# Kernel optimization log

Hardware: AMD Instinct MI355X
Metric: run time of the kernel (lower is better)

The kernel has to match this reference:

```python
import jax, jax.numpy as jnp
import numpy as np

D = 32          # latent_dimension
N = 100000      # num nodes
E = 3200000     # num edges (avg degree 32)
K = 4           # message-passing steps
GAMMA = 0.9
ALPHA = 0.5


def _lin(key, out_f, in_f):
    s = 1.0 / np.sqrt(in_f)
    kw, kb = jax.random.split(key)
    W = jax.random.uniform(kw, (out_f, in_f), minval=-s, maxval=s, dtype=jnp.float32)
    b = jax.random.uniform(kb, (out_f,), minval=-s, maxval=s, dtype=jnp.float32)
    return W, b


def setup_inputs() -> dict:
    key = jax.random.key(0)
    k = iter(jax.random.split(key, 32))
    inp = {}
    inp['x'] = jax.random.normal(next(k), (N, 3), dtype=jnp.float32)
    inp['y'] = jax.random.normal(next(k), (N, 2), dtype=jnp.float32)
    inp['edge_index'] = jax.random.randint(next(k), (2, E), 0, N)
    inp['edge_attr'] = jax.random.uniform(next(k), (E, 2), dtype=jnp.float32)
    inp['to_W1'], inp['to_b1'] = _lin(next(k), D, 2 * D + 2)
    inp['to_W2'], inp['to_b2'] = _lin(next(k), D, D)
    inp['fr_W1'], inp['fr_b1'] = _lin(next(k), D, 2 * D + 2)
    inp['fr_W2'], inp['fr_b2'] = _lin(next(k), D, D)
    inp['lp_W1'], inp['lp_b1'] = _lin(next(k), D, 2 * D + 1)
    inp['lp_W2'], inp['lp_b2'] = _lin(next(k), D, D)
    inp['gru_Wih'], inp['gru_bih'] = _lin(next(k), 3 * D, 4 * D + 3)
    inp['gru_Whh'], inp['gru_bhh'] = _lin(next(k), 3 * D, D)
    inp['dec_W1'], inp['dec_b1'] = _lin(next(k), D, D)
    inp['dec_W2'], inp['dec_b2'] = _lin(next(k), 2, D)
    return inp


def _mlp2(h, W1, b1, W2, b2):
    return jax.nn.relu(h @ W1.T + b1) @ W2.T + b2


def reference(x, y, edge_index, edge_attr,
              to_W1, to_b1, to_W2, to_b2,
              fr_W1, fr_b1, fr_W2, fr_b2,
              lp_W1, lp_b1, lp_W2, lp_b2,
              gru_Wih, gru_bih, gru_Whh, gru_bhh,
              dec_W1, dec_b1, dec_W2, dec_b2):
    n = x.shape[0]
    d = gru_Whh.shape[1]
    src, dst = edge_index[0], edge_index[1]
    nonself = src != dst                     # remove_self_loops in Phi modules
    emask = nonself.astype(x.dtype)          # [E]

    # Loop module: add_self_loops(weight=1), adjacency diagonal = 1 + sum of
    # original self-loop weights (edge_attr[:,0]); loop_col = 1 - diag.
    diag = jnp.ones((n,), x.dtype).at[src].add(
        jnp.where(nonself, jnp.zeros_like(edge_attr[:, 0]), edge_attr[:, 0]))
    loop_col = (1.0 - diag)[:, None]         # [N,1]

    def agg_mean(msg, idx):
        # masked scatter-mean over edges -> nodes; nodes w/o messages get 0
        s = jax.ops.segment_sum(msg * emask[:, None], idx, num_segments=n)
        c = jax.ops.segment_sum(emask, idx, num_segments=n)
        return s / jnp.maximum(c, 1.0)[:, None]

    def gru_step(xin):  # single-step GRU, h0 = 0 (W_hh @ h vanishes)
        g = xin @ gru_Wih.T + gru_bih
        r_x, z_x, n_x = jnp.split(g, 3, axis=-1)
        b_hr, b_hz, b_hn = jnp.split(gru_bhh, 3)
        r = jax.nn.sigmoid(r_x + b_hr)
        z = jax.nn.sigmoid(z_x + b_hz)
        nn_ = jnp.tanh(n_x + r * b_hn)
        return (1.0 - z) * nn_

    def decode(H):
        return _mlp2(H, dec_W1, dec_b1, dec_W2, dec_b2)

    H = jnp.zeros((n, d), x.dtype)
    losses = []
    F = decode(H)
    for _ in range(K):
        h_dst, h_src = H[dst], H[src]
        # Phi_to: flow source_to_target -> x_i = x[dst], x_j = x[src], agg @ dst
        m_to = agg_mean(_mlp2(jnp.concatenate([h_dst, h_src, edge_attr], 1),
                              to_W1, to_b1, to_W2, to_b2), dst)
        # Phi_from: flow target_to_source -> x_i = x[src], x_j = x[dst], agg @ src
        m_fr = agg_mean(_mlp2(jnp.concatenate([h_src, h_dst, edge_attr], 1),
                              fr_W1, fr_b1, fr_W2, fr_b2), src)
        lp = _mlp2(jnp.concatenate([H, H, loop_col], 1), lp_W1, lp_b1, lp_W2, lp_b2)
        concat = jnp.concatenate([H, m_to, m_fr, lp, x], 1)   # [N, 4D+3]
        H = gru_step(concat) * ALPHA + H
        F = decode(H)
        losses.append(jnp.mean((F - y) ** 2))
    losses = jnp.stack(losses)                                # [K]
    weights = GAMMA ** jnp.arange(K - 1, -1, -1, dtype=x.dtype)
    total_loss = jnp.sum(losses * weights)
    return F, total_loss, losses
```

## Files before the change

### kernel.cpp

```cpp
#include <hip/hip_runtime.h>
#include <math.h>


#define BSHIFT 9
#define BIN_W 512
#define CAP 17408
#define EPB 8192

__device__ __forceinline__ unsigned int pack_bf(float x) {
  unsigned int u = __float_as_uint(x);
  u += 0x7fffu + ((u >> 16) & 1u);
  return u >> 16;
}

__global__ void combine_kernel(const float* __restrict__ Wih, const float* __restrict__ bih,
    const float* __restrict__ toW2, const float* __restrict__ tob2,
    const float* __restrict__ frW2, const float* __restrict__ frb2,
    const float* __restrict__ lpW2, const float* __restrict__ lpb2,
    const float* __restrict__ lpW1,
    float* __restrict__ Wg, float* __restrict__ Wlp1c) {
  int tid = blockIdx.x * blockDim.x + threadIdx.x;
  if (tid < 9216) {
    int seg = tid / 3072, r2 = tid % 3072, g = r2 >> 5, j = r2 & 31;
    const float* W2 = seg == 0 ? toW2 : (seg == 1 ? frW2 : lpW2);
    const float* wrow = Wih + g*131 + 32 + seg*32;
    float s = 0.f;
    #pragma unroll
    for (int k = 0; k < 32; k++) s += wrow[k] * W2[k*32 + j];
    int nr = (g & 31)*3 + (g >> 5);
    Wg[nr*136 + 32 + seg*32 + j] = s;
  } else if (tid < 12288) {
    int r2 = tid - 9216, g = r2 >> 5, k = r2 & 31;
    int nr = (g & 31)*3 + (g >> 5);
    Wg[nr*136 + k] = Wih[g*131 + k];
  } else if (tid < 12576) {
    int r2 = tid - 12288; int g = r2 / 3, c = r2 % 3;
    int nr = (g & 31)*3 + (g >> 5);
    Wg[nr*136 + 128 + c] = Wih[g*131 + 128 + c];
  } else if (tid < 12672) {
    int g = tid - 12576;
    float vt = 0.f, vf = 0.f, bl = 0.f;
    #pragma unroll
    for (int k = 0; k < 32; k++) {
      vt += Wih[g*131 + 32 + k] * tob2[k];
      vf += Wih[g*131 + 64 + k] * frb2[k];
      bl += Wih[g*131 + 96 + k] * lpb2[k];
    }
    int nr = (g & 31)*3 + (g >> 5);
    Wg[nr*136 + 131] = bih[g] + bl;
    Wg[nr*136 + 132] = vt;
    Wg[nr*136 + 133] = vf;
  } else if (tid < 13696) {
    int r2 = tid - 12672; int i = r2 >> 5, k = r2 & 31;
    Wlp1c[i*32 + k] = lpW1[i*65 + k] + lpW1[i*65 + 32 + k];
  }
}

__global__ __launch_bounds__(256) void transpose_kernel(
    const float* __restrict__ Wg, const float* __restrict__ toW1,
    const float* __restrict__ frW1, const float* __restrict__ Wlp1c,
    const float* __restrict__ lpW1, const float* __restrict__ lpb1,
    float* __restrict__ Wgt, float* __restrict__ Wc, float* __restrict__ Wtail) {
  int tid = blockIdx.x*256 + threadIdx.x;
  if (tid < 12864) {
    int og = tid / 3216, r = tid % 3216, k = r / 24, jj = r % 24;
    Wgt[(og*134 + k)*32 + jj] = Wg[(og*24 + jj)*136 + k];
  } else if (tid < 12864 + 5120) {
    int r = tid - 12864;
    int og = r / 1280, r2 = r % 1280, k = r2 / 40, j = r2 % 40;
    int f = og*8 + (j & 7);
    int cls = j >> 3;
    float v;
    if      (cls == 0) v = toW1[f*66 + k];
    else if (cls == 1) v = toW1[f*66 + 32 + k];
    else if (cls == 2) v = frW1[f*66 + k];
    else if (cls == 3) v = frW1[f*66 + 32 + k];
    else               v = Wlp1c[f*32 + k];
    Wc[(og*32 + k)*48 + j] = v;
  } else if (tid < 12864 + 5120 + 64) {
    int f = tid - 12864 - 5120;
    Wtail[f] = (f < 32) ? lpW1[f*65 + 64] : lpb1[f - 32];
  }
}

__global__ __launch_bounds__(1024) void scatter_bin_kernel(
    const int* __restrict__ ei, const float* __restrict__ ea,
    int* __restrict__ cursor_to, int* __restrict__ cursor_fr,
    uint2* __restrict__ binned_to, uint2* __restrict__ binned_fr,
    float* __restrict__ loop_col, int E) {
  __shared__ int lh_to[256], lh_fr[256];
  __shared__ int gb_to[256], gb_fr[256];
  int t = threadIdx.x;
  if (t < 256) { lh_to[t] = 0; lh_fr[t] = 0; }
  __syncthreads();
  int base_e = blockIdx.x * EPB;
  #pragma unroll
  for (int j = 0; j < EPB/1024; j++) {
    int e = base_e + j*1024 + t;
    if (e < E) {
      int ss = ei[e], dd = ei[E + e];
      if (ss != dd) {
        atomicAdd(&lh_to[dd >> BSHIFT], 1);
        atomicAdd(&lh_fr[ss >> BSHIFT], 1);
      } else {
        atomicAdd(&loop_col[ss], -ea[2*e]);
      }
    }
  }
  __syncthreads();
  if (t < 256) {
    int c = lh_to[t]; gb_to[t] = c ? atomicAdd(&cursor_to[t], c) : 0; lh_to[t] = 0;
    c = lh_fr[t];     gb_fr[t] = c ? atomicAdd(&cursor_fr[t], c) : 0; lh_fr[t] = 0;
  }
  __syncthreads();
  #pragma unroll
  for (int j = 0; j < EPB/1024; j++) {
    int e = base_e + j*1024 + t;
    if (e < E) {
      int ss = ei[e], dd = ei[E + e];
      if (ss != dd) {
        float2 a = ((const float2*)ea)[e];
        unsigned int ep = pack_bf(a.x) | (pack_bf(a.y) << 16);
        int bt = dd >> BSHIFT, bf = ss >> BSHIFT;
        int st = gb_to[bt] + atomicAdd(&lh_to[bt], 1);
        int sf = gb_fr[bf] + atomicAdd(&lh_fr[bf], 1);
        if (st < CAP) binned_to[(size_t)bt*CAP + st] =
            make_uint2((unsigned int)ss | ((unsigned int)(dd & 511) << 17), ep);
        if (sf < CAP) binned_fr[(size_t)bf*CAP + sf] =
            make_uint2((unsigned int)dd | ((unsigned int)(ss & 511) << 17), ep);
      }
    }
  }
}

__global__ __launch_bounds__(256) void bin_count_kernel(
    const uint2* __restrict__ binned_to, const int* __restrict__ cursor_to,
    const uint2* __restrict__ binned_fr, const int* __restrict__ cursor_fr,
    int* __restrict__ cnt_dst, int* __restrict__ cnt_src, int NB, int N) {
  __shared__ int c[BIN_W];
  int b = blockIdx.x;
  bool second = b >= NB;
  if (second) b -= NB;
  const uint2* binned = second ? binned_fr : binned_to;
  const int* cursor   = second ? cursor_fr : cursor_to;
  int* cnt            = second ? cnt_src   : cnt_dst;
  for (int i = threadIdx.x; i < BIN_W; i += 256) c[i] = 0;
  __syncthreads();
  int m = cursor[b]; if (m > CAP) m = CAP;
  const uint2* seg = binned + (size_t)b*CAP;
  for (int i = threadIdx.x; i < m; i += 256)
    atomicAdd(&c[seg[i].x >> 17], 1);
  __syncthreads();
  for (int i = threadIdx.x; i < BIN_W; i += 256) {
    int n = (b << BSHIFT) + i;
    if (n < N) cnt[n] = c[i];
  }
}

__global__ __launch_bounds__(256) void scan_part_kernel(
    const int* __restrict__ cnt_a, const int* __restrict__ cnt_b,
    int* __restrict__ part, int n, int G) {
  __shared__ int ws[4];
  int b = blockIdx.x, t = threadIdx.x, lane = t & 63, w = t >> 6;
  int base = b*1024 + t*4;
  for (int which = 0; which < 2; which++) {
    const int* cnt = which ? cnt_b : cnt_a;
    int sum = 0;
    #pragma unroll
    for (int j = 0; j < 4; j++) if (base + j < n) sum += cnt[base + j];
    #pragma unroll
    for (int off = 32; off; off >>= 1) sum += __shfl_down(sum, off, 64);
    if (lane == 0) ws[w] = sum;
    __syncthreads();
    if (t == 0) part[which*G + b] = ws[0] + ws[1] + ws[2] + ws[3];
    __syncthreads();
  }
}

__global__ __launch_bounds__(256) void scan_mid_kernel(
    int* __restrict__ part, int* __restrict__ row_a, int* __restrict__ row_b,
    int n, int G) {
  __shared__ int ws[2][4];
  int t = threadIdx.x, lane = t & 63, w = t >> 6;
  for (int which = 0; which < 2; which++) {
    int v = (t < G) ? part[which*G + t] : 0;
    int orig = v;
    #pragma unroll
    for (int off = 1; off < 64; off <<= 1) {
      int u = __shfl_up(v, off, 64);
      if (lane >= off) v += u;
    }
    if (lane == 63) ws[which][w] = v;
    __syncthreads();
    int wadd = 0;
    for (int i = 0; i < w; i++) wadd += ws[which][i];
    int incl = v + wadd;
    if (t < G) part[which*G + t] = incl - orig;
    if (t == G - 1) { int* row = which ? row_b : row_a; row[n] = incl; }
    __syncthreads();
  }
}

__global__ __launch_bounds__(256) void scan_apply_kernel(
    const int* __restrict__ cnt_a, const int* __restrict__ cnt_b,
    const int* __restrict__ part, int* __restrict__ row_a, int* __restrict__ row_b,
    int n, int G) {
  __shared__ int ws[4];
  int b = blockIdx.x, t = threadIdx.x, lane = t & 63, w = t >> 6;
  int base = b*1024 + t*4;
  for (int which = 0; which < 2; which++) {
    const int* cnt = which ? cnt_b : cnt_a;
    int* row = which ? row_b : row_a;
    int v0 = (base   < n) ? cnt[base]   : 0;
    int v1 = (base+1 < n) ? cnt[base+1] : 0;
    int v2 = (base+2 < n) ? cnt[base+2] : 0;
    int v3 = (base+3 < n) ? cnt[base+3] : 0;
    int tsum = v0 + v1 + v2 + v3;
    int v = tsum;
    #pragma unroll
    for (int off = 1; off < 64; off <<= 1) {
      int u = __shfl_up(v, off, 64);
      if (lane >= off) v += u;
    }
    if (lane == 63) ws[w] = v;
    __syncthreads();
    int wadd = 0;
    for (int i = 0; i < w; i++) wadd += ws[i];
    int excl = v - tsum + wadd + part[which*G + b];
    if (base   < n) row[base]   = excl;
    if (base+1 < n) row[base+1] = excl + v0;
    if (base+2 < n) row[base+2] = excl + v0 + v1;
    if (base+3 < n) row[base+3] = excl + v0 + v1 + v2;
    __syncthreads();
  }
}

__global__ __launch_bounds__(256) void place_kernel(
    const uint2* __restrict__ binned_to, const int* __restrict__ cursor_to,
    const uint2* __restrict__ binned_fr, const int* __restrict__ cursor_fr,
    const int* __restrict__ row_to, const int* __restrict__ row_fr,
    uint2* __restrict__ rec_to, uint2* __restrict__ rec_fr, int NB, int N) {
  __shared__ int cur[BIN_W];
  int b = blockIdx.x;
  bool second = b >= NB;
  if (second) b -= NB;
  const uint2* binned = second ? binned_fr : binned_to;
  const int* cursor   = second ? cursor_fr : cursor_to;
  const int* row      = second ? row_fr    : row_to;
  uint2* rec          = second ? rec_fr    : rec_to;
  int n0 = b << BSHIFT;
  for (int i = threadIdx.x; i < BIN_W; i += 256) {
    int n = n0 + i;
    cur[i] = (n < N) ? row[n] : 0;
  }
  __syncthreads();
  int m = cursor[b]; if (m > CAP) m = CAP;
  const uint2* seg = binned + (size_t)b*CAP;
  for (int i = threadIdx.x; i < m; i += 256) {
    uint2 r = seg[i];
    int pos = atomicAdd(&cur[r.x >> 17], 1);
    rec[pos] = make_uint2((r.x & 0x1ffffu) << 5, r.y);
  }
}

__global__ __launch_bounds__(256) void hlp0_kernel(
    const float* __restrict__ lpW1, const float* __restrict__ lpb1,
    const float* __restrict__ loop_col, float* __restrict__ inX, int N) {
  int tid = blockIdx.x*256 + threadIdx.x;
  int n = tid >> 5, f = tid & 31;
  if (n < N)
    inX[(size_t)n*128 + 96 + f] = fmaxf(lpW1[f*65 + 64]*loop_col[n] + lpb1[f], 0.f);
}

__global__ __launch_bounds__(256) void agg_dual_kernel(
    const float* __restrict__ Pti, const unsigned short* __restrict__ Ptj,
    const int* __restrict__ row_to, const uint2* __restrict__ rec_to,
    const float* __restrict__ toW1, const float* __restrict__ tob1,
    const float* __restrict__ Pfi, const unsigned short* __restrict__ Pfj,
    const int* __restrict__ row_fr, const uint2* __restrict__ rec_fr,
    const float* __restrict__ frW1, const float* __restrict__ frb1,
    float* __restrict__ inX, int skipP, int N) {
  int b = blockIdx.x;
  int low = b & 7;
  bool second = low >= 4;
  int inner = (b >> 3)*4 + (low & 3);
  const float* Pi            = second ? Pfi   : Pti;
  const unsigned short* Pj   = second ? Pfj   : Ptj;
  const int* row             = second ? row_fr: row_to;
  const uint2* rec           = second ? rec_fr: rec_to;
  const float* W1            = second ? frW1  : toW1;
  const float* b1            = second ? frb1  : tob1;
  int slot                   = second ? 64    : 32;
  int t = inner*256 + threadIdx.x;
  int n = t >> 5;
  if (n >= N) return;
  int f = t & 31;
  int start = row[n], end = row[n+1];
  float we0 = W1[f*66 + 64], we1 = W1[f*66 + 65];
  float s = 0.f;
  const uint2* rp = rec + start;
  if (skipP) {
    float base = b1[f];
    #pragma unroll 8
    for (int i = start; i < end; i++) {
      uint2 r = *rp++;
      float e0 = __uint_as_float((r.y & 0xffffu) << 16);
      float e1 = __uint_as_float(r.y & 0xffff0000u);
      s += fmaxf(base + we0*e0 + we1*e1, 0.f);
    }
  } else {
    const unsigned short* Pjf = Pj + f;
    float base = Pi[n*32 + f] + b1[f];
    #pragma unroll 8
    for (int i = start; i < end; i++) {
      uint2 r = *rp++;
      float e0 = __uint_as_float((r.y & 0xffffu) << 16);
      float e1 = __uint_as_float(r.y & 0xffff0000u);
      float pj = __uint_as_float(((unsigned int)Pjf[r.x]) << 16);
      s += fmaxf(base + pj + we0*e0 + we1*e1, 0.f);
    }
  }
  int c = end - start;
  inX[(size_t)n*128 + slot + f] = s / (float)(c > 0 ? c : 1);
}

__global__ __launch_bounds__(256, 4) void node_update_kernel(
    float* __restrict__ inX, const float* __restrict__ Wgt,
    const float* __restrict__ x, const float* __restrict__ y,
    const int* __restrict__ cnt_dst, const int* __restrict__ cnt_src,
    const float* __restrict__ bhh,
    const float* __restrict__ dW1, const float* __restrict__ db1,
    const float* __restrict__ dW2, const float* __restrict__ db2,
    const float* __restrict__ loop_col,
    const float* __restrict__ Wc, const float* __restrict__ Wtail,
    float* __restrict__ Pti, unsigned short* __restrict__ Ptj,
    float* __restrict__ Pfi, unsigned short* __restrict__ Pfj,
    float* __restrict__ Fout, float* __restrict__ loss_acc, int k_iter, int N) {
  __shared__ float sbuf[64*137];
  __shared__ float sF[512];
  int t = threadIdx.x;
  int node0 = blockIdx.x * 64;
  {
    const float4* src = (const float4*)(inX + (size_t)node0*128);
    int nvalid = N - node0; if (nvalid > 64) nvalid = 64;
    int nfl4 = nvalid * 32;
    for (int i = t; i < 64*32; i += 256) {
      float4 v = (i < nfl4) ? src[i] : make_float4(0.f, 0.f, 0.f, 0.f);
      int node = i >> 5, k = (i & 31) * 4;
      float* dp = &sbuf[node*137 + k];
      dp[0] = v.x; dp[1] = v.y; dp[2] = v.z; dp[3] = v.w;
    }
    if (t < 64) {
      int n = node0 + t;
      float x0=0.f, x1=0.f, x2=0.f, gt=0.f, gf=0.f;
      if (n < N) {
        x0 = x[n*3]; x1 = x[n*3+1]; x2 = x[n*3+2];
        gt = cnt_dst[n] > 0 ? 1.f : 0.f;
        gf = cnt_src[n] > 0 ? 1.f : 0.f;
      }
      float* dp = &sbuf[t*137 + 128];
      dp[0]=x0; dp[1]=x1; dp[2]=x2; dp[3]=1.f; dp[4]=gt; dp[5]=gf;
    }
  }
  __syncthreads();
  int lane_node = t & 63;
  int og = __builtin_amdgcn_readfirstlane(t >> 6);
  const float* inrow = &sbuf[lane_node*137];
  float acc[24];
  #pragma unroll
  for (int jj = 0; jj < 24; jj++) acc[jj] = 0.f;
  const float* wt = Wgt + og*134*32;
  #pragma unroll 2
  for (int k = 0; k < 134; k++) {
    float iv = inrow[k];
    const float* wk = wt + k*32;
    #pragma unroll
    for (int jj = 0; jj < 24; jj++) acc[jj] += wk[jj] * iv;
  }
  float hnew[8];
  {
    int n = node0 + lane_node;
    #pragma unroll
    for (int q = 0; q < 8; q++) {
      int f = og*8 + q;
      float r = 1.f/(1.f + __expf(-(acc[q*3]   + bhh[f])));
      float z = 1.f/(1.f + __expf(-(acc[q*3+1] + bhh[32+f])));
      float nn = tanhf(acc[q*3+2] + r*bhh[64+f]);
      hnew[q] = (1.f - z)*nn*0.5f + inrow[f];
      if (n < N) inX[(size_t)n*128 + f] = hnew[q];
    }
  }
  __syncthreads();
  #pragma unroll
  for (int q = 0; q < 8; q++) sbuf[lane_node*137 + og*8 + q] = hnew[q];
  __syncthreads();
  float hn[32];
  #pragma unroll
  for (int k = 0; k < 32; k++) hn[k] = inrow[k];
  float F0p = 0.f, F1p = 0.f;
  #pragma unroll
  for (int q = 0; q < 8; q++) {
    int jd = og*8 + q;
    float a = db1[jd];
    const float* wd = dW1 + jd*32;
    #pragma unroll
    for (int k = 0; k < 32; k++) a += wd[k]*hn[k];
    a = fmaxf(a, 0.f);
    F0p += dW2[jd]*a;
    F1p += dW2[32+jd]*a;
  }
  sF[t*2] = F0p; sF[t*2+1] = F1p;
  __syncthreads();
  if (k_iter < 3) {
    int n = node0 + lane_node;
    bool valid = n < N;
    float lc = valid ? loop_col[n] : 0.f;
    int fb = og*8;
    float a[40];
    #pragma unroll
    for (int j = 0; j < 40; j++) a[j] = 0.f;
    const float* wc = Wc + og*32*48;
    #pragma unroll 2
    for (int k = 0; k < 32; k++) {
      float hk = hn[k];
      const float* wck = wc + k*48;
      #pragma unroll
      for (int j = 0; j < 40; j++) a[j] += wck[j] * hk;
    }
    if (valid) {
      float4* dp = (float4*)&Pti[(size_t)n*32 + fb];
      dp[0] = make_float4(a[0],a[1],a[2],a[3]);
      dp[1] = make_float4(a[4],a[5],a[6],a[7]);
      uint4 u;
      u.x = pack_bf(a[8])  | (pack_bf(a[9])  << 16);
      u.y = pack_bf(a[10]) | (pack_bf(a[11]) << 16);
      u.z = pack_bf(a[12]) | (pack_bf(a[13]) << 16);
      u.w = pack_bf(a[14]) | (pack_bf(a[15]) << 16);
      *(uint4*)&Ptj[(size_t)n*32 + fb] = u;
      dp = (float4*)&Pfi[(size_t)n*32 + fb];
      dp[0] = make_float4(a[16],a[17],a[18],a[19]);
      dp[1] = make_float4(a[20],a[21],a[22],a[23]);
      u.x = pack_bf(a[24]) | (pack_bf(a[25]) << 16);
      u.y = pack_bf(a[26]) | (pack_bf(a[27]) << 16);
      u.z = pack_bf(a[28]) | (pack_bf(a[29]) << 16);
      u.w = pack_bf(a[30]) | (pack_bf(a[31]) << 16);
      *(uint4*)&Pfj[(size_t)n*32 + fb] = u;
      float hl[8];
      #pragma unroll
      for (int q = 0; q < 8; q++)
        hl[q] = fmaxf(a[32+q] + Wtail[fb+q]*lc + Wtail[32+fb+q], 0.f);
      dp = (float4*)&inX[(size_t)n*128 + 96 + fb];
      dp[0] = make_float4(hl[0],hl[1],hl[2],hl[3]);
      dp[1] = make_float4(hl[4],hl[5],hl[6],hl[7]);
    }
  }
  float my_loss = 0.f;
  if (og == 0) {
    int n = node0 + lane_node;
    float F0 = db2[0] + sF[t*2]   + sF[(t+64)*2]   + sF[(t+128)*2]   + sF[(t+192)*2];
    float F1 = db2[1] + sF[t*2+1] + sF[(t+64)*2+1] + sF[(t+128)*2+1] + sF[(t+192)*2+1];
    if (n < N) {
      ((float2*)Fout)[n] = make_float2(F0, F1);
      float e0 = F0 - y[n*2], e1 = F1 - y[n*2+1];
      my_loss = e0*e0 + e1*e1;
    }
  }
  #pragma unroll
  for (int off = 32; off > 0; off >>= 1) my_loss += __shfl_down(my_loss, off, 64);
  if (t == 0) atomicAdd(&loss_acc[k_iter], my_loss);
}

__global__ void finalize_kernel(const float* __restrict__ loss_acc, float* __restrict__ out, int N) {
  if (threadIdx.x == 0 && blockIdx.x == 0) {
    float inv = 1.f/(2.f*(float)N);
    float l0 = loss_acc[0]*inv, l1 = loss_acc[1]*inv, l2 = loss_acc[2]*inv, l3 = loss_acc[3]*inv;
    out[0] = l0*0.729f + l1*0.81f + l2*0.9f + l3;
    out[1] = l0; out[2] = l1; out[3] = l2; out[4] = l3;
  }
}

extern "C" void kernel_launch(void* const* d_in, const int* in_sizes, int n_in,
                              void* d_out, int out_size, void* d_ws, size_t ws_size,
                              hipStream_t stream) {
  const float* x    = (const float*)d_in[0];
  const float* y    = (const float*)d_in[1];
  const int*   ei   = (const int*)  d_in[2];
  const float* ea   = (const float*)d_in[3];
  const float* toW1 = (const float*)d_in[4];  const float* tob1 = (const float*)d_in[5];
  const float* toW2 = (const float*)d_in[6];  const float* tob2 = (const float*)d_in[7];
  const float* frW1 = (const float*)d_in[8];  const float* frb1 = (const float*)d_in[9];
  const float* frW2 = (const float*)d_in[10]; const float* frb2 = (const float*)d_in[11];
  const float* lpW1 = (const float*)d_in[12]; const float* lpb1 = (const float*)d_in[13];
  const float* lpW2 = (const float*)d_in[14]; const float* lpb2 = (const float*)d_in[15];
  const float* gWih = (const float*)d_in[16]; const float* gbih = (const float*)d_in[17];
  const float* gbhh = (const float*)d_in[19];
  const float* dW1  = (const float*)d_in[20]; const float* db1  = (const float*)d_in[21];
  const float* dW2  = (const float*)d_in[22]; const float* db2  = (const float*)d_in[23];
  const int N = in_sizes[0] / 3;
  const int E = in_sizes[3] / 2;
  const int NB = (N + BIN_W - 1) >> BSHIFT;
  const int G  = (N + 1023) >> 10;

  char* p = (char*)d_ws;
  auto carve = [&](size_t bytes) -> void* {
    void* r = (void*)p;
    p += (bytes + 255) & ~(size_t)255;
    return r;
  };
  float* inX       = (float*)carve((size_t)N*128*4);
  float* loop_col  = (float*)carve((size_t)N*4);
  int*   cursor_to = (int*)  carve((size_t)NB*4);
  int*   cursor_fr = (int*)  carve((size_t)NB*4);
  float* loss_acc  = (float*)carve(64);
  size_t zero_bytes = (size_t)(p - (char*)d_ws);
  int*    row_to   = (int*)  carve((size_t)(N+1)*4);
  int*    row_fr   = (int*)  carve((size_t)(N+1)*4);
  int*    cnt_dst  = (int*)  carve((size_t)N*4);
  int*    cnt_src  = (int*)  carve((size_t)N*4);
  int*    part     = (int*)  carve((size_t)2*G*4);
  uint2*  binned_to= (uint2*)carve((size_t)NB*CAP*8);
  uint2*  binned_fr= (uint2*)carve((size_t)NB*CAP*8);
  uint2*  rec_to   = (uint2*)carve((size_t)E*8);
  uint2*  rec_fr   = (uint2*)carve((size_t)E*8);
  float*  Pti      = (float*)carve((size_t)N*32*4);
  float*  Pfi      = (float*)carve((size_t)N*32*4);
  unsigned short* Ptj = (unsigned short*)carve((size_t)N*32*2);
  unsigned short* Pfj = (unsigned short*)carve((size_t)N*32*2);
  float*  Wg       = (float*)carve((size_t)96*136*4);
  float*  Wlp1c    = (float*)carve(32*32*4);
  float*  Wgt      = (float*)carve((size_t)4*134*32*4);
  float*  Wc       = (float*)carve((size_t)4*32*48*4);
  float*  Wtail    = (float*)carve(64*4);

  hipMemsetAsync(d_ws, 0, zero_bytes, stream);
  combine_kernel<<<54, 256, 0, stream>>>(gWih, gbih, toW2, tob2, frW2, frb2, lpW2, lpb2,
                                         lpW1, Wg, Wlp1c);
  transpose_kernel<<<71, 256, 0, stream>>>(Wg, toW1, frW1, Wlp1c, lpW1, lpb1,
                                           Wgt, Wc, Wtail);
  scatter_bin_kernel<<<(E+EPB-1)/EPB, 1024, 0, stream>>>(ei, ea, cursor_to, cursor_fr,
                                                         binned_to, binned_fr, loop_col, E);
  bin_count_kernel<<<2*NB, 256, 0, stream>>>(binned_to, cursor_to, binned_fr, cursor_fr,
                                             cnt_dst, cnt_src, NB, N);
  scan_part_kernel<<<G, 256, 0, stream>>>(cnt_dst, cnt_src, part, N, G);
  scan_mid_kernel<<<1, 256, 0, stream>>>(part, row_to, row_fr, N, G);
  scan_apply_kernel<<<G, 256, 0, stream>>>(cnt_dst, cnt_src, part, row_to, row_fr, N, G);
  place_kernel<<<2*NB, 256, 0, stream>>>(binned_to, cursor_to, binned_fr, cursor_fr,
                                         row_to, row_fr, rec_to, rec_fr, NB, N);
  hlp0_kernel<<<(N*32 + 255)/256, 256, 0, stream>>>(lpW1, lpb1, loop_col, inX, N);

  float* Fout     = (float*)d_out;
  float* loss_out = (float*)d_out + (size_t)N*2;

  int aggHalf = (N*32 + 255)/256;
  int aggHalf4 = (aggHalf + 3) & ~3;
  for (int k = 0; k < 4; k++) {
    agg_dual_kernel<<<2*aggHalf4, 256, 0, stream>>>(Pti, Ptj, row_to, rec_to, toW1, tob1,
                                                    Pfi, Pfj, row_fr, rec_fr, frW1, frb1,
                                                    inX, (k == 0) ? 1 : 0, N);
    node_update_kernel<<<(N+63)/64, 256, 0, stream>>>(inX, Wgt, x, y,
        cnt_dst, cnt_src, gbhh, dW1, db1, dW2, db2,
        loop_col, Wc, Wtail,
        Pti, Ptj, Pfi, Pfj, Fout, loss_acc, k, N);
  }
  finalize_kernel<<<1, 64, 0, stream>>>(loss_acc, loss_out, N);
}
```

Measured before the change: 1.109 ms.

## Split neighbor gather into two passes by neighbor-index half for cache locality

The CSR rows are split into two sub-segments per node according to whether the neighbor index falls in the lower or upper half of the node range. Aggregation then runs as two passes, each touching only half of the bf16 Pj table, so the random gathers fit better in cache. The first pass stores partial sums and the second pass reloads them, adds its own part and divides by the degree. This costs an extra kernel launch, an extra read-modify-write of the aggregate slots, and twice as many entries in the count and scan arrays.

Measured after the change: 1.328 ms. 1.2x slower.

```diff
diff --git a/kernel.cpp b/kernel.cpp
--- a/kernel.cpp
+++ b/kernel.cpp
@@ -136,24 +136,28 @@
 __global__ __launch_bounds__(256) void bin_count_kernel(
     const uint2* __restrict__ binned_to, const int* __restrict__ cursor_to,
     const uint2* __restrict__ binned_fr, const int* __restrict__ cursor_fr,
-    int* __restrict__ cnt_dst, int* __restrict__ cnt_src, int NB, int N) {
-  __shared__ int c[BIN_W];
+    int* __restrict__ cnt2_dst, int* __restrict__ cnt2_src, int NB, int N) {
+  __shared__ int c[2*BIN_W];
   int b = blockIdx.x;
   bool second = b >= NB;
   if (second) b -= NB;
   const uint2* binned = second ? binned_fr : binned_to;
   const int* cursor   = second ? cursor_fr : cursor_to;
-  int* cnt            = second ? cnt_src   : cnt_dst;
-  for (int i = threadIdx.x; i < BIN_W; i += 256) c[i] = 0;
+  int* cnt2           = second ? cnt2_src  : cnt2_dst;
+  int Nh = N >> 1;
+  for (int i = threadIdx.x; i < 2*BIN_W; i += 256) c[i] = 0;
   __syncthreads();
   int m = cursor[b]; if (m > CAP) m = CAP;
   const uint2* seg = binned + (size_t)b*CAP;
-  for (int i = threadIdx.x; i < m; i += 256)
-    atomicAdd(&c[seg[i].x >> 17], 1);
-  __syncthreads();
-  for (int i = threadIdx.x; i < BIN_W; i += 256) {
-    int n = (b << BSHIFT) + i;
-    if (n < N) cnt[n] = c[i];
+  for (int i = threadIdx.x; i < m; i += 256) {
+    unsigned int rx = seg[i].x;
+    int h = ((rx & 0x1ffffu) >= (unsigned)Nh) ? 1 : 0;
+    atomicAdd(&c[((rx >> 17) << 1) + h], 1);
+  }
+  __syncthreads();
+  for (int j = threadIdx.x; j < 2*BIN_W; j += 256) {
+    int n = (b << BSHIFT) + (j >> 1);
+    if (n < N) cnt2[((size_t)n << 1) + (j & 1)] = c[j];
   }
 }
 
@@ -238,27 +242,29 @@
 __global__ __launch_bounds__(256) void place_kernel(
     const uint2* __restrict__ binned_to, const int* __restrict__ cursor_to,
     const uint2* __restrict__ binned_fr, const int* __restrict__ cursor_fr,
-    const int* __restrict__ row_to, const int* __restrict__ row_fr,
+    const int* __restrict__ row2_to, const int* __restrict__ row2_fr,
     uint2* __restrict__ rec_to, uint2* __restrict__ rec_fr, int NB, int N) {
-  __shared__ int cur[BIN_W];
+  __shared__ int cur[2*BIN_W];
   int b = blockIdx.x;
   bool second = b >= NB;
   if (second) b -= NB;
   const uint2* binned = second ? binned_fr : binned_to;
   const int* cursor   = second ? cursor_fr : cursor_to;
-  const int* row      = second ? row_fr    : row_to;
+  const int* row2     = second ? row2_fr   : row2_to;
   uint2* rec          = second ? rec_fr    : rec_to;
+  int Nh = N >> 1;
   int n0 = b << BSHIFT;
-  for (int i = threadIdx.x; i < BIN_W; i += 256) {
-    int n = n0 + i;
-    cur[i] = (n < N) ? row[n] : 0;
+  for (int j = threadIdx.x; j < 2*BIN_W; j += 256) {
+    int n = n0 + (j >> 1);
+    cur[j] = (n < N) ? row2[((size_t)n << 1) + (j & 1)] : 0;
   }
   __syncthreads();
   int m = cursor[b]; if (m > CAP) m = CAP;
   const uint2* seg = binned + (size_t)b*CAP;
   for (int i = threadIdx.x; i < m; i += 256) {
     uint2 r = seg[i];
-    int pos = atomicAdd(&cur[r.x >> 17], 1);
+    int h = ((r.x & 0x1ffffu) >= (unsigned)Nh) ? 1 : 0;
+    int pos = atomicAdd(&cur[((r.x >> 17) << 1) + h], 1);
     rec[pos] = make_uint2((r.x & 0x1ffffu) << 5, r.y);
   }
 }
@@ -274,60 +280,71 @@
 
 __global__ __launch_bounds__(256) void agg_dual_kernel(
     const float* __restrict__ Pti, const unsigned short* __restrict__ Ptj,
-    const int* __restrict__ row_to, const uint2* __restrict__ rec_to,
+    const int* __restrict__ row2_to, const uint2* __restrict__ rec_to,
     const float* __restrict__ toW1, const float* __restrict__ tob1,
     const float* __restrict__ Pfi, const unsigned short* __restrict__ Pfj,
-    const int* __restrict__ row_fr, const uint2* __restrict__ rec_fr,
+    const int* __restrict__ row2_fr, const uint2* __restrict__ rec_fr,
     const float* __restrict__ frW1, const float* __restrict__ frb1,
-    float* __restrict__ inX, int skipP, int N) {
+    float* __restrict__ inX, int pass, int N) {
   int b = blockIdx.x;
   int low = b & 7;
   bool second = low >= 4;
   int inner = (b >> 3)*4 + (low & 3);
-  const float* Pi            = second ? Pfi   : Pti;
-  const unsigned short* Pj   = second ? Pfj   : Ptj;
-  const int* row             = second ? row_fr: row_to;
-  const uint2* rec           = second ? rec_fr: rec_to;
-  const float* W1            = second ? frW1  : toW1;
-  const float* b1            = second ? frb1  : tob1;
-  int slot                   = second ? 64    : 32;
+  const float* Pi            = second ? Pfi    : Pti;
+  const unsigned short* Pj   = second ? Pfj    : Ptj;
+  const int* row2            = second ? row2_fr: row2_to;
+  const uint2* rec           = second ? rec_fr : rec_to;
+  const float* W1            = second ? frW1   : toW1;
+  const float* b1            = second ? frb1   : tob1;
+  int slot                   = second ? 64     : 32;
   int t = inner*256 + threadIdx.x;
   int n = t >> 5;
   if (n >= N) return;
   int f = t & 31;
-  int start = row[n], end = row[n+1];
+  int r0 = row2[2*n], r1 = row2[2*n+1], r2v = row2[2*n+2];
   float we0 = W1[f*66 + 64], we1 = W1[f*66 + 65];
   float s = 0.f;
-  const uint2* rp = rec + start;
-  if (skipP) {
+  size_t oidx = (size_t)n*128 + slot + f;
+  if (pass == 2) {
     float base = b1[f];
+    const uint2* rp = rec + r0;
     #pragma unroll 8
-    for (int i = start; i < end; i++) {
+    for (int i = r0; i < r2v; i++) {
       uint2 r = *rp++;
       float e0 = __uint_as_float((r.y & 0xffffu) << 16);
       float e1 = __uint_as_float(r.y & 0xffff0000u);
       s += fmaxf(base + we0*e0 + we1*e1, 0.f);
     }
+    int c = r2v - r0;
+    inX[oidx] = s / (float)(c > 0 ? c : 1);
+    return;
+  }
+  const unsigned short* Pjf = Pj + f;
+  float base = Pi[n*32 + f] + b1[f];
+  int g0 = pass ? r1 : r0;
+  int g1 = pass ? r2v : r1;
+  const uint2* rp = rec + g0;
+  #pragma unroll 8
+  for (int i = g0; i < g1; i++) {
+    uint2 r = *rp++;
+    float e0 = __uint_as_float((r.y & 0xffffu) << 16);
+    float e1 = __uint_as_float(r.y & 0xffff0000u);
+    float pj = __uint_as_float(((unsigned int)Pjf[r.x]) << 16);
+    s += fmaxf(base + pj + we0*e0 + we1*e1, 0.f);
+  }
+  if (pass == 0) {
+    __builtin_nontemporal_store(s, &inX[oidx]);
   } else {
-    const unsigned short* Pjf = Pj + f;
-    float base = Pi[n*32 + f] + b1[f];
-    #pragma unroll 8
-    for (int i = start; i < end; i++) {
-      uint2 r = *rp++;
-      float e0 = __uint_as_float((r.y & 0xffffu) << 16);
-      float e1 = __uint_as_float(r.y & 0xffff0000u);
-      float pj = __uint_as_float(((unsigned int)Pjf[r.x]) << 16);
-      s += fmaxf(base + pj + we0*e0 + we1*e1, 0.f);
-    }
-  }
-  int c = end - start;
-  inX[(size_t)n*128 + slot + f] = s / (float)(c > 0 ? c : 1);
+    s += __builtin_nontemporal_load(&inX[oidx]);
+    int c = r2v - r0;
+    inX[oidx] = s / (float)(c > 0 ? c : 1);
+  }
 }
 
 __global__ __launch_bounds__(256, 4) void node_update_kernel(
     float* __restrict__ inX, const float* __restrict__ Wgt,
     const float* __restrict__ x, const float* __restrict__ y,
-    const int* __restrict__ cnt_dst, const int* __restrict__ cnt_src,
+    const int* __restrict__ row2_to, const int* __restrict__ row2_fr,
     const float* __restrict__ bhh,
     const float* __restrict__ dW1, const float* __restrict__ db1,
     const float* __restrict__ dW2, const float* __restrict__ db2,
@@ -355,8 +372,8 @@
       float x0=0.f, x1=0.f, x2=0.f, gt=0.f, gf=0.f;
       if (n < N) {
         x0 = x[n*3]; x1 = x[n*3+1]; x2 = x[n*3+2];
-        gt = cnt_dst[n] > 0 ? 1.f : 0.f;
-        gf = cnt_src[n] > 0 ? 1.f : 0.f;
+        gt = (row2_to[2*n+2] > row2_to[2*n]) ? 1.f : 0.f;
+        gf = (row2_fr[2*n+2] > row2_fr[2*n]) ? 1.f : 0.f;
       }
       float* dp = &sbuf[t*137 + 128];
       dp[0]=x0; dp[1]=x1; dp[2]=x2; dp[3]=1.f; dp[4]=gt; dp[5]=gf;
@@ -499,7 +516,8 @@
   const int N = in_sizes[0] / 3;
   const int E = in_sizes[3] / 2;
   const int NB = (N + BIN_W - 1) >> BSHIFT;
-  const int G  = (N + 1023) >> 10;
+  const int N2 = 2*N;
+  const int G2 = (N2 + 1023) >> 10;
 
   char* p = (char*)d_ws;
   auto carve = [&](size_t bytes) -> void* {
@@ -513,11 +531,11 @@
   int*   cursor_fr = (int*)  carve((size_t)NB*4);
   float* loss_acc  = (float*)carve(64);
   size_t zero_bytes = (size_t)(p - (char*)d_ws);
-  int*    row_to   = (int*)  carve((size_t)(N+1)*4);
-  int*    row_fr   = (int*)  carve((size_t)(N+1)*4);
-  int*    cnt_dst  = (int*)  carve((size_t)N*4);
-  int*    cnt_src  = (int*)  carve((size_t)N*4);
-  int*    part     = (int*)  carve((size_t)2*G*4);
+  int*    row2_to  = (int*)  carve((size_t)(N2+1)*4);
+  int*    row2_fr  = (int*)  carve((size_t)(N2+1)*4);
+  int*    cnt2_dst = (int*)  carve((size_t)N2*4);
+  int*    cnt2_src = (int*)  carve((size_t)N2*4);
+  int*    part     = (int*)  carve((size_t)2*G2*4);
   uint2*  binned_to= (uint2*)carve((size_t)NB*CAP*8);
   uint2*  binned_fr= (uint2*)carve((size_t)NB*CAP*8);
   uint2*  rec_to   = (uint2*)carve((size_t)E*8);
@@ -540,12 +558,12 @@
   scatter_bin_kernel<<<(E+EPB-1)/EPB, 1024, 0, stream>>>(ei, ea, cursor_to, cursor_fr,
                                                          binned_to, binned_fr, loop_col, E);
   bin_count_kernel<<<2*NB, 256, 0, stream>>>(binned_to, cursor_to, binned_fr, cursor_fr,
-                                             cnt_dst, cnt_src, NB, N);
-  scan_part_kernel<<<G, 256, 0, stream>>>(cnt_dst, cnt_src, part, N, G);
-  scan_mid_kernel<<<1, 256, 0, stream>>>(part, row_to, row_fr, N, G);
-  scan_apply_kernel<<<G, 256, 0, stream>>>(cnt_dst, cnt_src, part, row_to, row_fr, N, G);
+                                             cnt2_dst, cnt2_src, NB, N);
+  scan_part_kernel<<<G2, 256, 0, stream>>>(cnt2_dst, cnt2_src, part, N2, G2);
+  scan_mid_kernel<<<1, 256, 0, stream>>>(part, row2_to, row2_fr, N2, G2);
+  scan_apply_kernel<<<G2, 256, 0, stream>>>(cnt2_dst, cnt2_src, part, row2_to, row2_fr, N2, G2);
   place_kernel<<<2*NB, 256, 0, stream>>>(binned_to, cursor_to, binned_fr, cursor_fr,
-                                         row_to, row_fr, rec_to, rec_fr, NB, N);
+                                         row2_to, row2_fr, rec_to, rec_fr, NB, N);
   hlp0_kernel<<<(N*32 + 255)/256, 256, 0, stream>>>(lpW1, lpb1, loop_col, inX, N);
 
   float* Fout     = (float*)d_out;
@@ -554,13 +572,22 @@
   int aggHalf = (N*32 + 255)/256;
   int aggHalf4 = (aggHalf + 3) & ~3;
   for (int k = 0; k < 4; k++) {
-    agg_dual_kernel<<<2*aggHalf4, 256, 0, stream>>>(Pti, Ptj, row_to, rec_to, toW1, tob1,
-                                                    Pfi, Pfj, row_fr, rec_fr, frW1, frb1,
-                                                    inX, (k == 0) ? 1 : 0, N);
+    if (k == 0) {
+      agg_dual_kernel<<<2*aggHalf4, 256, 0, stream>>>(Pti, Ptj, row2_to, rec_to, toW1, tob1,
+                                                      Pfi, Pfj, row2_fr, rec_fr, frW1, frb1,
+                                                      inX, 2, N);
+    } else {
+      agg_dual_kernel<<<2*aggHalf4, 256, 0, stream>>>(Pti, Ptj, row2_to, rec_to, toW1, tob1,
+                                                      Pfi, Pfj, row2_fr, rec_fr, frW1, frb1,
+                                                      inX, 0, N);
+      agg_dual_kernel<<<2*aggHalf4, 256, 0, stream>>>(Pti, Ptj, row2_to, rec_to, toW1, tob1,
+                                                      Pfi, Pfj, row2_fr, rec_fr, frW1, frb1,
+                                                      inX, 1, N);
+    }
     node_update_kernel<<<(N+63)/64, 256, 0, stream>>>(inX, Wgt, x, y,
-        cnt_dst, cnt_src, gbhh, dW1, db1, dW2, db2,
+        row2_to, row2_fr, gbhh, dW1, db1, dW2, db2,
         loop_col, Wc, Wtail,
         Pti, Ptj, Pfi, Pfj, Fout, loss_acc, k, N);
-  }
+    }
   finalize_kernel<<<1, 64, 0, stream>>>(loss_acc, loss_out, N);
 }
```
